# Optimization experiments

Measured on AMD Instinct MI355X. Metric: run time of the kernel, lower is better.

## Reference

```python
import jax, jax.numpy as jnp
import numpy as np

N = 100000      # total nodes (100 graphs x 1000 nodes each)
G = 100         # graphs per batch
F_IN = 12       # node_features (temporal window)
F_OUT = 32      # DCRNN hidden size (hardcoded in module)
K = 5           # diffusion (Chebyshev) steps (hardcoded)
C = 4           # num_classes
E = 16 * N      # edges: ring (N) + random (15N)


def setup_inputs() -> dict:
    key = jax.random.key(0)
    ks = jax.random.split(key, 12)
    x = jax.random.normal(ks[0], (N, F_IN), dtype=jnp.float32)
    ring = jnp.arange(N, dtype=jnp.int32)
    src = jnp.concatenate([ring, jax.random.randint(ks[1], (15 * N,), 0, N, dtype=jnp.int32)])
    dst = jnp.concatenate([(ring + 1) % N, jax.random.randint(ks[2], (15 * N,), 0, N, dtype=jnp.int32)])
    edge_index = jnp.stack([src, dst])  # [2, E]
    edge_weight = jax.random.uniform(ks[3], (E,), dtype=jnp.float32, minval=0.1, maxval=1.0)
    batch = (jnp.arange(N, dtype=jnp.int32) * G) // N  # sorted graph ids, 1000 nodes per graph
    s = 0.1
    return dict(
        x=x, edge_index=edge_index, edge_weight=edge_weight, batch=batch,
        W_z=jax.random.normal(ks[4], (2, K, F_IN + F_OUT, F_OUT), jnp.float32) * s,
        b_z=jax.random.normal(ks[5], (F_OUT,), jnp.float32) * s,
        W_r=jax.random.normal(ks[6], (2, K, F_IN + F_OUT, F_OUT), jnp.float32) * s,
        b_r=jax.random.normal(ks[7], (F_OUT,), jnp.float32) * s,
        W_h=jax.random.normal(ks[8], (2, K, F_IN + F_OUT, F_OUT), jnp.float32) * s,
        b_h=jax.random.normal(ks[9], (F_OUT,), jnp.float32) * s,
        W_lin=jax.random.normal(ks[10], (F_OUT, C), jnp.float32) * s,
        b_lin=jax.random.normal(ks[11], (C,), jnp.float32) * s,
    )


def reference(x, edge_index, edge_weight, batch, W_z, b_z, W_r, b_r, W_h, b_h, W_lin, b_lin):
    row, col = edge_index[0], edge_index[1]
    # weighted in/out degrees (to_dense_adj sums duplicate edges, same as segment_sum)
    deg_out_inv = 1.0 / jax.ops.segment_sum(edge_weight, row, num_segments=N)
    deg_in_inv = 1.0 / jax.ops.segment_sum(edge_weight, col, num_segments=N)
    norm_out = deg_out_inv[row][:, None]  # per-edge 1/deg_out(src)
    norm_in = deg_in_inv[row][:, None]    # per-edge 1/deg_in(src), as in DConv

    def prop_fwd(h):  # out[dst] += h[src]/deg_out[src]
        return jax.ops.segment_sum(norm_out * h[row], col, num_segments=N)

    def prop_rev(h):  # reverse (transposed) diffusion: out[src] += h[dst]/deg_in[src]
        return jax.ops.segment_sum(norm_in * h[col], row, num_segments=N)

    def dconv(Xc, W, b):
        # Chebyshev diffusion conv, W: [2, K, F_in+F_out, F_out]
        H = Xc @ (W[0, 0] + W[1, 0])
        T1o, T1i = prop_fwd(Xc), prop_rev(Xc)
        H = H + T1o @ W[0, 1] + T1i @ W[1, 1]
        T0o = T0i = Xc
        for k in range(2, K):
            T2o = 2.0 * prop_fwd(T1o) - T0o
            T2i = 2.0 * prop_rev(T1i) - T0i
            H = H + T2o @ W[0, k] + T2i @ W[1, k]
            T0o, T1o = T1o, T2o
            T0i, T1i = T1i, T2i
        return H + b

    # GRU gating with zero-initialized hidden state (H=None in module)
    Hst = jnp.zeros((N, F_OUT), x.dtype)
    XH = jnp.concatenate([x, Hst], axis=1)
    Z = jax.nn.sigmoid(dconv(XH, W_z, b_z))
    R = jax.nn.sigmoid(dconv(XH, W_r, b_r))
    XRH = jnp.concatenate([x, R * Hst], axis=1)
    H_tilde = jnp.tanh(dconv(XRH, W_h, b_h))
    H = Z * Hst + (1.0 - Z) * H_tilde

    h = jax.nn.relu(H) @ W_lin + b_lin            # [N, C]
    sums = jax.ops.segment_sum(h, batch, num_segments=G)
    counts = jax.ops.segment_sum(jnp.ones((N,), h.dtype), batch, num_segments=G)
    return sums / counts[:, None]                 # global_mean_pool -> [G, C]
```

## Files before the change

### kernel.cpp

```cpp
#include <hip/hip_runtime.h>
#include <math.h>

#define NN    100000
#define GG    100
#define FIN   12
#define FOUT  32
#define KD    5
#define CC    4
#define EE    1600000
#define ROWS  108
#define NBF   782
#define NBINS 1564
#define NBC   512
#define CHUNK 3125
#define TOTR  (2 * CHUNK)
#define NSEG  (NBINS * NBC)
#define SUBMAX 3072

__device__ __forceinline__ unsigned bfr(float f) {
    unsigned u = __float_as_uint(f);
    return (u + 0x7FFFu + ((u >> 16) & 1u)) >> 16;
}
__device__ __forceinline__ unsigned pack2(float a, float b) {
    return bfr(a) | (bfr(b) << 16);
}
#define BLO(u) __uint_as_float((u) << 16)
#define BHI(u) __uint_as_float((u) & 0xFFFF0000u)

__device__ __forceinline__ int chunk_of_block(int b) {
    return ((b & 7) << 6) | (b >> 3);
}


__global__ __launch_bounds__(512) void k_hist(const int* __restrict__ ei,
                                              int* __restrict__ hist_g) {
    __shared__ int hist[NBINS];
    for (int i = threadIdx.x; i < NBINS; i += 512) hist[i] = 0;
    __syncthreads();
    int chunk = chunk_of_block(blockIdx.x);
    int lo = chunk * CHUNK, hi = lo + CHUNK;
    for (int e = lo + threadIdx.x; e < hi; e += 512) {
        int s = ei[e], d = ei[EE + e];
        atomicAdd(&hist[d >> 7], 1);
        atomicAdd(&hist[NBF + (s >> 7)], 1);
    }
    __syncthreads();
    for (int i = threadIdx.x; i < NBINS; i += 512)
        hist_g[i * NBC + chunk] = hist[i];
}

__global__ __launch_bounds__(1024) void k_scan1(
        int* __restrict__ g, int* __restrict__ bsum,
        const float* __restrict__ Wz_in, const float* __restrict__ Wh_in,
        float* __restrict__ Wz, float* __restrict__ Wh,
        const float* __restrict__ b_lin, float* __restrict__ out,
        const float* __restrict__ x, uint2* __restrict__ xb) {
    __shared__ int sh[1024];
    int t = threadIdx.x;
    int i = blockIdx.x * 1024 + t;
    int v = g[i];
    sh[t] = v;
    __syncthreads();
    for (int d = 1; d < 1024; d <<= 1) {
        int x2 = sh[t];
        if (t >= d) x2 += sh[t - d];
        __syncthreads();
        sh[t] = x2;
        __syncthreads();
    }
    g[i] = sh[t] - v;
    if (t == 1023) bsum[blockIdx.x] = sh[1023];

    if (i < 2 * ROWS * FOUT) {
        int sel = i / (ROWS * FOUT);
        int rem = i - sel * ROWS * FOUT;
        int r = rem / FOUT;
        int f = rem - r * FOUT;
        int b = r / 12;
        int ii = r - b * 12;
        const float* Ws = sel ? Wh_in : Wz_in;
        float vv;
        if (b == 0)
            vv = Ws[(0 * KD + 0) * 44 * 32 + ii * 32 + f] + Ws[(1 * KD + 0) * 44 * 32 + ii * 32 + f];
        else if (b <= 4)
            vv = Ws[(0 * KD + b) * 44 * 32 + ii * 32 + f];
        else
            vv = Ws[(1 * KD + (b - 4)) * 44 * 32 + ii * 32 + f];
        (sel ? Wh : Wz)[r * FOUT + f] = vv;
    }
    int u = i - 2 * ROWS * FOUT;
    if (u >= 0 && u < GG * CC) out[u] = b_lin[u & 3];
    if (i < 3 * NN) {
        int n = i / 3, c = i - n * 3;
        float4 vf = *(const float4*)(x + (size_t)n * FIN + c * 4);
        xb[(size_t)n * 3 + c] = make_uint2(pack2(vf.x, vf.y), pack2(vf.z, vf.w));
    }
}

__global__ __launch_bounds__(1024) void k_scan3(int* __restrict__ g,
                                                const int* __restrict__ bsum,
                                                int* __restrict__ off,
                                                int* __restrict__ off_node) {
    __shared__ int sh[1024];
    int t = threadIdx.x;
    sh[t] = (t < blockIdx.x) ? bsum[t] : 0;
    __syncthreads();
    for (int d = 512; d > 0; d >>= 1) {
        if (t < d) sh[t] += sh[t + d];
        __syncthreads();
    }
    int base = sh[0];
    int i = blockIdx.x * 1024 + t;
    int v = g[i] + base;
    g[i] = v;
    if ((i & (NBC - 1)) == 0) off[i / NBC] = v;
    if (i == 0) { off[NBINS] = 2 * EE; off_node[2 * NN] = 2 * EE; }
}

__global__ __launch_bounds__(512) void k_place(const int* __restrict__ ei,
                                               const float* __restrict__ ew,
                                               const int* __restrict__ base_g,
                                               int2* __restrict__ recA) {
    __shared__ int2 ldsrec[TOTR];
    __shared__ int  lofs[NBINS];
    __shared__ int  cur[NBINS];
    __shared__ int  sbase[NBINS];
    __shared__ unsigned short binof[TOTR];
    int* psum = (int*)binof;
    int t = threadIdx.x;
    int chunk = chunk_of_block(blockIdx.x);

    for (int bin = t; bin < NBINS; bin += 512) {
        int b0 = base_g[bin * NBC + chunk];
        int b1;
        if (chunk < NBC - 1)      b1 = base_g[bin * NBC + chunk + 1];
        else if (bin < NBINS - 1) b1 = base_g[(bin + 1) * NBC];
        else                      b1 = 2 * EE;
        sbase[bin] = b0;
        lofs[bin] = b1 - b0;
        cur[bin] = 0;
    }
    __syncthreads();

    int i0 = t * 4;
    int v0 = 0, v1 = 0, v2 = 0, v3 = 0;
    if (i0 + 0 < NBINS) v0 = lofs[i0];
    if (i0 + 1 < NBINS) v1 = lofs[i0 + 1];
    if (i0 + 2 < NBINS) v2 = lofs[i0 + 2];
    if (i0 + 3 < NBINS) v3 = lofs[i0 + 3];
    int s = v0 + v1 + v2 + v3;
    psum[t] = s;
    __syncthreads();
    for (int d = 1; d < 512; d <<= 1) {
        int x = psum[t];
        if (t >= d) x += psum[t - d];
        __syncthreads();
        psum[t] = x;
        __syncthreads();
    }
    int run = psum[t] - s;
    __syncthreads();
    if (i0 + 0 < NBINS) { lofs[i0]     = run; run += v0; }
    if (i0 + 1 < NBINS) { lofs[i0 + 1] = run; run += v1; }
    if (i0 + 2 < NBINS) { lofs[i0 + 2] = run; run += v2; }
    if (i0 + 3 < NBINS) { lofs[i0 + 3] = run; run += v3; }
    __syncthreads();

    int lo = chunk * CHUNK;
    for (int e = lo + t; e < lo + CHUNK; e += 512) {
        int s2 = ei[e], d2 = ei[EE + e];
        float w = ew[e];
        int bf = d2 >> 7;
        int pf = lofs[bf] + atomicAdd(&cur[bf], 1);
        ldsrec[pf] = make_int2(s2 | ((d2 & 127) << 17), __float_as_int(w));
        binof[pf] = (unsigned short)bf;
        int br = NBF + (s2 >> 7);
        int pr = lofs[br] + atomicAdd(&cur[br], 1);
        ldsrec[pr] = make_int2(d2 | ((s2 & 127) << 17), __float_as_int(w));
        binof[pr] = (unsigned short)br;
    }
    __syncthreads();

    for (int i = t; i < TOTR; i += 512) {
        int b = binof[i];
        recA[sbase[b] + (i - lofs[b])] = ldsrec[i];
    }
}

__global__ __launch_bounds__(256) void k_subcsr(
        const int* __restrict__ off, const int2* __restrict__ recA,
        const float* __restrict__ x,
        int* __restrict__ off_node, int* __restrict__ rec2,
        float* __restrict__ dinv_in, float* __restrict__ dinv_out,
        uint2* __restrict__ gA) {
    __shared__ int2  seg[SUBMAX];
    __shared__ int   hist[128];
    __shared__ int   lofs[128];
    __shared__ int   cur[128];
    __shared__ float wsum[128];
    __shared__ float dl[128];
    int b = blockIdx.x;
    int t = threadIdx.x;
    if (t < 128) { hist[t] = 0; wsum[t] = 0.f; }
    __syncthreads();
    int e0 = off[b], e1 = off[b + 1];
    int cnt = e1 - e0;
    bool stg = (cnt <= SUBMAX);
    if (stg) {
        for (int i = t; i < cnt; i += 256) {
            int2 r = recA[e0 + i];
            seg[i] = r;
            int loc = r.x >> 17;
            atomicAdd(&hist[loc], 1);
            atomicAdd(&wsum[loc], __int_as_float(r.y));
        }
    } else {
        for (int i = t; i < cnt; i += 256) {
            int2 r = recA[e0 + i];
            int loc = r.x >> 17;
            atomicAdd(&hist[loc], 1);
            atomicAdd(&wsum[loc], __int_as_float(r.y));
        }
    }
    __syncthreads();
    if (t < 128) lofs[t] = hist[t];
    __syncthreads();
    for (int d = 1; d < 128; d <<= 1) {
        int v = 0;
        if (t < 128 && t >= d) v = lofs[t - d];
        __syncthreads();
        if (t < 128) lofs[t] += v;
        __syncthreads();
    }
    bool rev = b >= NBF;
    int base = (rev ? b - NBF : b) * 128;
    if (t < 128) {
        int ex = lofs[t] - hist[t];
        lofs[t] = ex;
        cur[t] = 0;
        int node = base + t;
        if (node < NN) {
            off_node[(rev ? NN : 0) + node] = e0 + ex;
            float inv = 1.f / wsum[t];
            dl[t] = inv;
            if (rev) dinv_out[node] = inv;
            else     dinv_in[node]  = inv;
        }
    }
    __syncthreads();
    if (stg) {
        for (int i = t; i < cnt; i += 256) {
            int rx = seg[i].x;
            int loc = rx >> 17;
            int pos = e0 + lofs[loc] + atomicAdd(&cur[loc], 1);
            rec2[pos] = rx & 0x1FFFF;
        }
    } else {
        for (int i = t; i < cnt; i += 256) {
            int rx = recA[e0 + i].x;
            int loc = rx >> 17;
            int pos = e0 + lofs[loc] + atomicAdd(&cur[loc], 1);
            rec2[pos] = rx & 0x1FFFF;
        }
    }
    if (rev) {
        __syncthreads();
        for (int i = t; i < 128 * 3; i += 256) {
            int loc = i / 3, cc = i - loc * 3;
            int node = base + loc;
            if (node < NN) {
                float4 v = *(const float4*)(x + (size_t)node * FIN + cc * 4);
                float sc = dl[loc];
                gA[(size_t)node * 3 + cc] =
                    make_uint2(pack2(v.x * sc, v.y * sc), pack2(v.z * sc, v.w * sc));
            }
        }
    }
}

#define LREC 2048
__global__ __launch_bounds__(256) void k_gather(
        const int* __restrict__ off_node, const int* __restrict__ rec2,
        const uint2* __restrict__ gIn, const uint2* __restrict__ hIn,
        const uint2* __restrict__ prevF, const uint2* __restrict__ prevR,
        const float* __restrict__ dinv_in, const float* __restrict__ dinv_out,
        uint2* __restrict__ outF, uint2* __restrict__ outR,
        uint2* __restrict__ gOut, float c) {
    __shared__ int lrec[LREC];
    int xcd = blockIdx.x & 7;
    int grp = blockIdx.x >> 3;
    bool rev = xcd >= 4;
    int dbase = rev ? NN : 0;
    int ub = (grp * 4 + (xcd & 3)) * 256;
    int lin = ub + threadIdx.x;

    int u1 = ub + 255; if (u1 > 3 * NN - 1) u1 = 3 * NN - 1;
    int node0 = ub / 3, node1 = u1 / 3;
    int w0 = off_node[dbase + node0];
    int w1 = off_node[dbase + node1 + 1];
    int wn = w1 - w0;
    bool useLds = (wn <= LREC);
    if (useLds) {
        for (int i = threadIdx.x; i < wn; i += 256) lrec[i] = rec2[w0 + i];
    }
    __syncthreads();

    if (lin < 3 * NN) {
        int node = lin / 3;
        int ch = lin - node * 3;
        int i0 = dbase + node;
        int e0 = off_node[i0], e1 = off_node[i0 + 1];
        const uint2* in = rev ? hIn : gIn;

        float ax = 0.f, ay = 0.f, az = 0.f, aw = 0.f;
        float bx = 0.f, by = 0.f, bz = 0.f, bw = 0.f;
        if (useLds) {
            int a0 = e0 - w0, a1 = e1 - w0;
            int e = a0;
            for (; e + 7 < a1; e += 8) {
                int n0 = lrec[e],     n1 = lrec[e + 1], n2 = lrec[e + 2], n3 = lrec[e + 3];
                int n4 = lrec[e + 4], n5 = lrec[e + 5], n6 = lrec[e + 6], n7 = lrec[e + 7];
                uint2 v0 = in[(size_t)n0 * 3 + ch];
                uint2 v1 = in[(size_t)n1 * 3 + ch];
                uint2 v2 = in[(size_t)n2 * 3 + ch];
                uint2 v3 = in[(size_t)n3 * 3 + ch];
                uint2 v4 = in[(size_t)n4 * 3 + ch];
                uint2 v5 = in[(size_t)n5 * 3 + ch];
                uint2 v6 = in[(size_t)n6 * 3 + ch];
                uint2 v7 = in[(size_t)n7 * 3 + ch];
                ax += BLO(v0.x); ay += BHI(v0.x); az += BLO(v0.y); aw += BHI(v0.y);
                bx += BLO(v1.x); by += BHI(v1.x); bz += BLO(v1.y); bw += BHI(v1.y);
                ax += BLO(v2.x); ay += BHI(v2.x); az += BLO(v2.y); aw += BHI(v2.y);
                bx += BLO(v3.x); by += BHI(v3.x); bz += BLO(v3.y); bw += BHI(v3.y);
                ax += BLO(v4.x); ay += BHI(v4.x); az += BLO(v4.y); aw += BHI(v4.y);
                bx += BLO(v5.x); by += BHI(v5.x); bz += BLO(v5.y); bw += BHI(v5.y);
                ax += BLO(v6.x); ay += BHI(v6.x); az += BLO(v6.y); aw += BHI(v6.y);
                bx += BLO(v7.x); by += BHI(v7.x); bz += BLO(v7.y); bw += BHI(v7.y);
            }
            for (; e < a1; ++e) {
                int n0 = lrec[e];
                uint2 v0 = in[(size_t)n0 * 3 + ch];
                ax += BLO(v0.x); ay += BHI(v0.x); az += BLO(v0.y); aw += BHI(v0.y);
            }
        } else {
            for (int e = e0; e < e1; ++e) {
                int n0 = rec2[e];
                uint2 v0 = in[(size_t)n0 * 3 + ch];
                ax += BLO(v0.x); ay += BHI(v0.x); az += BLO(v0.y); aw += BHI(v0.y);
            }
        }
        ax += bx; ay += by; az += bz; aw += bw;

        float sc = rev ? c * dinv_in[node] : c;
        ax *= sc; ay *= sc; az *= sc; aw *= sc;

        size_t o = (size_t)node * 3 + ch;
        if (prevF) {
            uint2 p = (rev ? prevR : prevF)[o];
            ax -= BLO(p.x); ay -= BHI(p.x); az -= BLO(p.y); aw -= BHI(p.y);
        }
        (rev ? outR : outF)[o] = make_uint2(pack2(ax, ay), pack2(az, aw));
        if (!rev && gOut) {
            float g = dinv_out[node];
            gOut[o] = make_uint2(pack2(g * ax, g * ay), pack2(g * az, g * aw));
        }
    }
}


#define SEGN  50
#define NSEGB 20
#define FREC  1280
__global__ __launch_bounds__(256) void k_fused(
        const float* __restrict__ x, const uint2* __restrict__ TS2,
        const int* __restrict__ off_node, const int* __restrict__ rec2,
        const uint2* __restrict__ gB, const float* __restrict__ dinv_in,
        const float* __restrict__ Wz, const float* __restrict__ Wh,
        const float* __restrict__ bz, const float* __restrict__ bh,
        const float* __restrict__ Wlin, float* __restrict__ out) {
    __shared__ float rows[64][13];
    __shared__ float red[256 * CC];
    __shared__ int   frec[FREC];
    int g = blockIdx.x / NSEGB;
    int seg = blockIdx.x - g * NSEGB;
    int base = g * 1000 + seg * SEGN;
    int tid = threadIdx.x;
    int lane = tid & 63;
    int wave = tid >> 6;
    int f0 = __builtin_amdgcn_readfirstlane(wave * 8);
    bool act = lane < SEGN;

    const uint2* T2o = TS2 + (size_t)1 * NN * 3;
    const uint2* T2i = TS2 + (size_t)5 * NN * 3;
    const uint2* T3i = TS2 + (size_t)6 * NN * 3;

    float az0[8], ah0[8];
#pragma unroll
    for (int fi = 0; fi < 8; ++fi) {
        az0[fi] = bz[f0 + fi];
        ah0[fi] = bh[f0 + fi];
    }

    for (int b = 0; b < 9; ++b) {
        __syncthreads();
        if (b == 0) {
            const float* src = x + (size_t)base * FIN;
            if (tid < 150) {
                float4 v = *(const float4*)(src + tid * 4);
                int e = tid * 4;
                int n0 = e / 12,       i0 = e - n0 * 12;       rows[n0][i0] = v.x;
                int n1 = (e + 1) / 12, i1 = (e + 1) - n1 * 12; rows[n1][i1] = v.y;
                int n2 = (e + 2) / 12, i2 = (e + 2) - n2 * 12; rows[n2][i2] = v.z;
                int n3 = (e + 3) / 12, i3 = (e + 3) - n3 * 12; rows[n3][i3] = v.w;
            }
        } else if (b == 4 || b == 8) {
            bool revd = (b == 8);
            int dbase = revd ? NN : 0;
            const uint2* gin  = revd ? T3i : gB;
            const uint2* prev = revd ? T2i : T2o;
            int w0 = off_node[dbase + base];
            int w1 = off_node[dbase + base + SEGN];
            int wn = w1 - w0;
            bool useLds = (wn <= FREC);
            if (useLds) {
                for (int i = tid; i < wn; i += 256) frec[i] = rec2[w0 + i];
            }
            __syncthreads();
            if (tid < 150) {
                int n = tid / 3, cc = tid - n * 3;
                int node = base + n;
                int e0 = off_node[dbase + node], e1 = off_node[dbase + node + 1];
                float ax = 0.f, ay = 0.f, az = 0.f, aw = 0.f;
                float bx2 = 0.f, by2 = 0.f, bz2 = 0.f, bw2 = 0.f;
                if (useLds) {
                    int a0 = e0 - w0, a1 = e1 - w0;
                    int e = a0;
                    for (; e + 7 < a1; e += 8) {
                        int n0 = frec[e],     n1 = frec[e + 1], n2 = frec[e + 2], n3 = frec[e + 3];
                        int n4 = frec[e + 4], n5 = frec[e + 5], n6 = frec[e + 6], n7 = frec[e + 7];
                        uint2 v0 = gin[(size_t)n0 * 3 + cc];
                        uint2 v1 = gin[(size_t)n1 * 3 + cc];
                        uint2 v2 = gin[(size_t)n2 * 3 + cc];
                        uint2 v3 = gin[(size_t)n3 * 3 + cc];
                        uint2 v4 = gin[(size_t)n4 * 3 + cc];
                        uint2 v5 = gin[(size_t)n5 * 3 + cc];
                        uint2 v6 = gin[(size_t)n6 * 3 + cc];
                        uint2 v7 = gin[(size_t)n7 * 3 + cc];
                        ax += BLO(v0.x); ay += BHI(v0.x); az += BLO(v0.y); aw += BHI(v0.y);
                        bx2 += BLO(v1.x); by2 += BHI(v1.x); bz2 += BLO(v1.y); bw2 += BHI(v1.y);
                        ax += BLO(v2.x); ay += BHI(v2.x); az += BLO(v2.y); aw += BHI(v2.y);
                        bx2 += BLO(v3.x); by2 += BHI(v3.x); bz2 += BLO(v3.y); bw2 += BHI(v3.y);
                        ax += BLO(v4.x); ay += BHI(v4.x); az += BLO(v4.y); aw += BHI(v4.y);
                        bx2 += BLO(v5.x); by2 += BHI(v5.x); bz2 += BLO(v5.y); bw2 += BHI(v5.y);
                        ax += BLO(v6.x); ay += BHI(v6.x); az += BLO(v6.y); aw += BHI(v6.y);
                        bx2 += BLO(v7.x); by2 += BHI(v7.x); bz2 += BLO(v7.y); bw2 += BHI(v7.y);
                    }
                    for (; e < a1; ++e) {
                        uint2 v = gin[(size_t)frec[e] * 3 + cc];
                        ax += BLO(v.x); ay += BHI(v.x); az += BLO(v.y); aw += BHI(v.y);
                    }
                } else {
                    for (int e = e0; e < e1; ++e) {
                        uint2 v = gin[(size_t)rec2[e] * 3 + cc];
                        ax += BLO(v.x); ay += BHI(v.x); az += BLO(v.y); aw += BHI(v.y);
                    }
                }
                ax += bx2; ay += by2; az += bz2; aw += bw2;
                float sc = revd ? 2.f * dinv_in[node] : 2.f;
                uint2 p = prev[(size_t)node * 3 + cc];
                rows[n][cc * 4 + 0] = ax * sc - BLO(p.x);
                rows[n][cc * 4 + 1] = ay * sc - BHI(p.x);
                rows[n][cc * 4 + 2] = az * sc - BLO(p.y);
                rows[n][cc * 4 + 3] = aw * sc - BHI(p.y);
            }
        } else {
            const uint2* Tb = TS2 + (size_t)(b - 1) * NN * 3;
            if (tid < 150) {
                int n = tid / 3, cc = tid - n * 3;
                uint2 v = Tb[(size_t)(base + n) * 3 + cc];
                rows[n][cc * 4 + 0] = BLO(v.x);
                rows[n][cc * 4 + 1] = BHI(v.x);
                rows[n][cc * 4 + 2] = BLO(v.y);
                rows[n][cc * 4 + 3] = BHI(v.y);
            }
        }
        __syncthreads();
        const float* wzr = Wz + b * 12 * FOUT + f0;
        const float* whr = Wh + b * 12 * FOUT + f0;
#pragma unroll
        for (int i = 0; i < FIN; ++i) {
            float v0 = rows[lane][i];
#pragma unroll
            for (int fi = 0; fi < 8; ++fi) {
                float wz = wzr[i * FOUT + fi];
                float wh = whr[i * FOUT + fi];
                az0[fi] = fmaf(v0, wz, az0[fi]);
                ah0[fi] = fmaf(v0, wh, ah0[fi]);
            }
        }
    }

    float o[CC] = {0.f, 0.f, 0.f, 0.f};
    if (act) {
#pragma unroll
        for (int fi = 0; fi < 8; ++fi) {
            float z = 1.f / (1.f + __expf(-az0[fi]));
            float e2 = __expf(2.f * ah0[fi]);
            float th = 1.f - 2.f / (e2 + 1.f);
            float hv = fmaxf((1.f - z) * th, 0.f);
#pragma unroll
            for (int c = 0; c < CC; ++c) o[c] = fmaf(hv, Wlin[(f0 + fi) * 4 + c], o[c]);
        }
    }

#pragma unroll
    for (int c = 0; c < CC; ++c) red[tid * CC + c] = o[c];
    __syncthreads();
    for (int st = 128; st > 0; st >>= 1) {
        if (tid < st) {
#pragma unroll
            for (int c = 0; c < CC; ++c) red[tid * CC + c] += red[(tid + st) * CC + c];
        }
        __syncthreads();
    }
    if (tid == 0) {
#pragma unroll
        for (int c = 0; c < CC; ++c) atomicAdd(out + g * CC + c, red[c] * 0.001f);
    }
}


extern "C" void kernel_launch(void* const* d_in, const int* in_sizes, int n_in,
                              void* d_out, int out_size, void* d_ws, size_t ws_size,
                              hipStream_t stream) {
    const float* x     = (const float*)d_in[0];
    const int*   ei    = (const int*)d_in[1];
    const float* ew    = (const float*)d_in[2];
    const float* W_z   = (const float*)d_in[4];
    const float* b_z   = (const float*)d_in[5];
    const float* W_h   = (const float*)d_in[8];
    const float* b_h   = (const float*)d_in[9];
    const float* W_lin = (const float*)d_in[10];
    const float* b_lin = (const float*)d_in[11];
    float* out = (float*)d_out;

    int*   rec2     = (int*)d_ws;
    unsigned* TSb   = (unsigned*)(rec2 + 2 * (size_t)EE);
    int2*  recA     = (int2*)TSb;
    int*   hist_g   = rec2;
    int*   bsumS    = rec2 + NSEG;
    unsigned* gAu   = TSb + (size_t)8 * NN * 6 + 1600000;
    unsigned* gBu   = gAu + (size_t)NN * 6;
    unsigned* xbu   = gBu + (size_t)NN * 6;
    float* dinv_in  = (float*)(xbu + (size_t)NN * 6);
    float* dinv_out = dinv_in + NN;
    float* Wz       = dinv_out + NN;
    float* Wh       = Wz + ROWS * FOUT;
    int*   off      = (int*)(Wh + ROWS * FOUT);
    int*   off_node = off + NBINS + 1;

    uint2* TS2 = (uint2*)TSb;
    uint2* T1o = TS2 + (size_t)0 * NN * 3;
    uint2* T2o = TS2 + (size_t)1 * NN * 3;
    uint2* T3o = TS2 + (size_t)2 * NN * 3;
    uint2* T1i = TS2 + (size_t)4 * NN * 3;
    uint2* T2i = TS2 + (size_t)5 * NN * 3;
    uint2* T3i = TS2 + (size_t)6 * NN * 3;
    uint2* gA = (uint2*)gAu;
    uint2* gB = (uint2*)gBu;
    uint2* xb = (uint2*)xbu;

    dim3 B(256);
    int nbG = 2344;
    int nbScan = NSEG / 1024;

    k_hist<<<NBC, 512, 0, stream>>>(ei, hist_g);
    k_scan1<<<nbScan, 1024, 0, stream>>>(hist_g, bsumS, W_z, W_h, Wz, Wh, b_lin, out, x, xb);
    k_scan3<<<nbScan, 1024, 0, stream>>>(hist_g, bsumS, off, off_node);
    k_place<<<NBC, 512, 0, stream>>>(ei, ew, hist_g, recA);
    k_subcsr<<<NBINS, B, 0, stream>>>(off, recA, x, off_node, rec2, dinv_in, dinv_out, gA);

    k_gather<<<nbG, B, 0, stream>>>(off_node, rec2, gA, xb,  nullptr, nullptr, dinv_in, dinv_out, T1o, T1i, gB, 1.f);
    k_gather<<<nbG, B, 0, stream>>>(off_node, rec2, gB, T1i, xb,      xb,      dinv_in, dinv_out, T2o, T2i, gA, 2.f);
    k_gather<<<nbG, B, 0, stream>>>(off_node, rec2, gA, T2i, T1o,     T1i,     dinv_in, dinv_out, T3o, T3i, gB, 2.f);

    k_fused<<<NSEGB * GG, B, 0, stream>>>(x, TS2, off_node, rec2, gB, dinv_in,
                                          Wz, Wh, b_z, b_h, W_lin, out);
}
```

Baseline: 299.9 us.

## Warp-specialize fused head kernel with producer/consumer double-buffered rows

The final fused kernel now uses 512-thread blocks covering 250 nodes instead of 50. Four producer waves load or gather the next basis block into one of two LDS row buffers while four consumer waves accumulate the projection for the current block, each consumer handling four nodes. This overlaps the gather latency with the FMA work, cuts the block count, and raises per-thread register use. The gather portion is spread over fewer total threads, which may limit parallelism in the memory-bound gather steps.

```diff
diff --git a/kernel.cpp b/kernel.cpp
--- a/kernel.cpp
+++ b/kernel.cpp
@@ -368,155 +368,178 @@
 }
 
 
-#define SEGN  50
-#define NSEGB 20
-#define FREC  1280
-__global__ __launch_bounds__(256) void k_fused(
+#define SEGN  250
+#define NSEGB 4
+#define FREC  5120
+__global__ __launch_bounds__(512) void k_fused(
         const float* __restrict__ x, const uint2* __restrict__ TS2,
         const int* __restrict__ off_node, const int* __restrict__ rec2,
         const uint2* __restrict__ gB, const float* __restrict__ dinv_in,
         const float* __restrict__ Wz, const float* __restrict__ Wh,
         const float* __restrict__ bz, const float* __restrict__ bh,
         const float* __restrict__ Wlin, float* __restrict__ out) {
-    __shared__ float rows[64][13];
-    __shared__ float red[256 * CC];
+    __shared__ float rows[2][256][13];
+    __shared__ float red[512 * CC];
     __shared__ int   frec[FREC];
-    int g = blockIdx.x / NSEGB;
-    int seg = blockIdx.x - g * NSEGB;
+    int g = blockIdx.x >> 2;
+    int seg = blockIdx.x & 3;
     int base = g * 1000 + seg * SEGN;
     int tid = threadIdx.x;
     int lane = tid & 63;
     int wave = tid >> 6;
-    int f0 = __builtin_amdgcn_readfirstlane(wave * 8);
-    bool act = lane < SEGN;
+    bool cons = wave < 4;
+    int pid = tid - 256;
+    int f0 = __builtin_amdgcn_readfirstlane((wave & 3) * 8);
 
     const uint2* T2o = TS2 + (size_t)1 * NN * 3;
     const uint2* T2i = TS2 + (size_t)5 * NN * 3;
     const uint2* T3i = TS2 + (size_t)6 * NN * 3;
 
-    float az0[8], ah0[8];
+    float az0[8], ah0[8], az1[8], ah1[8], az2[8], ah2[8], az3[8], ah3[8];
 #pragma unroll
     for (int fi = 0; fi < 8; ++fi) {
-        az0[fi] = bz[f0 + fi];
-        ah0[fi] = bh[f0 + fi];
-    }
+        float vz = bz[f0 + fi], vh = bh[f0 + fi];
+        az0[fi] = vz; ah0[fi] = vh; az1[fi] = vz; ah1[fi] = vh;
+        az2[fi] = vz; ah2[fi] = vh; az3[fi] = vz; ah3[fi] = vh;
+    }
+
+    if (!cons) {
+        const float* src = x + (size_t)base * FIN;
+        for (int q = pid; q < 750; q += 256) {
+            float4 v = *(const float4*)(src + q * 4);
+            int e = q * 4;
+            int n0 = e / 12,       i0 = e - n0 * 12;       rows[0][n0][i0] = v.x;
+            int n1 = (e + 1) / 12, i1 = (e + 1) - n1 * 12; rows[0][n1][i1] = v.y;
+            int n2 = (e + 2) / 12, i2 = (e + 2) - n2 * 12; rows[0][n2][i2] = v.z;
+            int n3 = (e + 3) / 12, i3 = (e + 3) - n3 * 12; rows[0][n3][i3] = v.w;
+        }
+    }
+    __syncthreads();
 
     for (int b = 0; b < 9; ++b) {
-        __syncthreads();
-        if (b == 0) {
-            const float* src = x + (size_t)base * FIN;
-            if (tid < 150) {
-                float4 v = *(const float4*)(src + tid * 4);
-                int e = tid * 4;
-                int n0 = e / 12,       i0 = e - n0 * 12;       rows[n0][i0] = v.x;
-                int n1 = (e + 1) / 12, i1 = (e + 1) - n1 * 12; rows[n1][i1] = v.y;
-                int n2 = (e + 2) / 12, i2 = (e + 2) - n2 * 12; rows[n2][i2] = v.z;
-                int n3 = (e + 3) / 12, i3 = (e + 3) - n3 * 12; rows[n3][i3] = v.w;
-            }
-        } else if (b == 4 || b == 8) {
-            bool revd = (b == 8);
+        int nb = b + 1;
+        int cur = b & 1, nxt = nb & 1;
+        if (nb == 4 || nb == 8) {
+            bool revd = (nb == 8);
             int dbase = revd ? NN : 0;
-            const uint2* gin  = revd ? T3i : gB;
-            const uint2* prev = revd ? T2i : T2o;
             int w0 = off_node[dbase + base];
             int w1 = off_node[dbase + base + SEGN];
             int wn = w1 - w0;
             bool useLds = (wn <= FREC);
             if (useLds) {
-                for (int i = tid; i < wn; i += 256) frec[i] = rec2[w0 + i];
+                for (int i = tid; i < wn; i += 512) frec[i] = rec2[w0 + i];
             }
             __syncthreads();
-            if (tid < 150) {
-                int n = tid / 3, cc = tid - n * 3;
-                int node = base + n;
-                int e0 = off_node[dbase + node], e1 = off_node[dbase + node + 1];
-                float ax = 0.f, ay = 0.f, az = 0.f, aw = 0.f;
-                float bx2 = 0.f, by2 = 0.f, bz2 = 0.f, bw2 = 0.f;
-                if (useLds) {
-                    int a0 = e0 - w0, a1 = e1 - w0;
-                    int e = a0;
-                    for (; e + 7 < a1; e += 8) {
-                        int n0 = frec[e],     n1 = frec[e + 1], n2 = frec[e + 2], n3 = frec[e + 3];
-                        int n4 = frec[e + 4], n5 = frec[e + 5], n6 = frec[e + 6], n7 = frec[e + 7];
-                        uint2 v0 = gin[(size_t)n0 * 3 + cc];
-                        uint2 v1 = gin[(size_t)n1 * 3 + cc];
-                        uint2 v2 = gin[(size_t)n2 * 3 + cc];
-                        uint2 v3 = gin[(size_t)n3 * 3 + cc];
-                        uint2 v4 = gin[(size_t)n4 * 3 + cc];
-                        uint2 v5 = gin[(size_t)n5 * 3 + cc];
-                        uint2 v6 = gin[(size_t)n6 * 3 + cc];
-                        uint2 v7 = gin[(size_t)n7 * 3 + cc];
-                        ax += BLO(v0.x); ay += BHI(v0.x); az += BLO(v0.y); aw += BHI(v0.y);
-                        bx2 += BLO(v1.x); by2 += BHI(v1.x); bz2 += BLO(v1.y); bw2 += BHI(v1.y);
-                        ax += BLO(v2.x); ay += BHI(v2.x); az += BLO(v2.y); aw += BHI(v2.y);
-                        bx2 += BLO(v3.x); by2 += BHI(v3.x); bz2 += BLO(v3.y); bw2 += BHI(v3.y);
-                        ax += BLO(v4.x); ay += BHI(v4.x); az += BLO(v4.y); aw += BHI(v4.y);
-                        bx2 += BLO(v5.x); by2 += BHI(v5.x); bz2 += BLO(v5.y); bw2 += BHI(v5.y);
-                        ax += BLO(v6.x); ay += BHI(v6.x); az += BLO(v6.y); aw += BHI(v6.y);
-                        bx2 += BLO(v7.x); by2 += BHI(v7.x); bz2 += BLO(v7.y); bw2 += BHI(v7.y);
+            if (!cons) {
+                const uint2* gin  = revd ? T3i : gB;
+                const uint2* prev = revd ? T2i : T2o;
+                for (int item = pid; item < 750; item += 256) {
+                    int n = item / 3, cc = item - n * 3;
+                    int node = base + n;
+                    int e0 = off_node[dbase + node], e1 = off_node[dbase + node + 1];
+                    float ax = 0.f, ay = 0.f, az = 0.f, aw = 0.f;
+                    float bx2 = 0.f, by2 = 0.f, bz2 = 0.f, bw2 = 0.f;
+                    if (useLds) {
+                        int a0 = e0 - w0, a1 = e1 - w0;
+                        int e = a0;
+                        for (; e + 7 < a1; e += 8) {
+                            int n0 = frec[e],     n1 = frec[e + 1], n2 = frec[e + 2], n3 = frec[e + 3];
+                            int n4 = frec[e + 4], n5 = frec[e + 5], n6 = frec[e + 6], n7 = frec[e + 7];
+                            uint2 v0 = gin[(size_t)n0 * 3 + cc];
+                            uint2 v1 = gin[(size_t)n1 * 3 + cc];
+                            uint2 v2 = gin[(size_t)n2 * 3 + cc];
+                            uint2 v3 = gin[(size_t)n3 * 3 + cc];
+                            uint2 v4 = gin[(size_t)n4 * 3 + cc];
+                            uint2 v5 = gin[(size_t)n5 * 3 + cc];
+                            uint2 v6 = gin[(size_t)n6 * 3 + cc];
+                            uint2 v7 = gin[(size_t)n7 * 3 + cc];
+                            ax += BLO(v0.x); ay += BHI(v0.x); az += BLO(v0.y); aw += BHI(v0.y);
+                            bx2 += BLO(v1.x); by2 += BHI(v1.x); bz2 += BLO(v1.y); bw2 += BHI(v1.y);
+                            ax += BLO(v2.x); ay += BHI(v2.x); az += BLO(v2.y); aw += BHI(v2.y);
+                            bx2 += BLO(v3.x); by2 += BHI(v3.x); bz2 += BLO(v3.y); bw2 += BHI(v3.y);
+                            ax += BLO(v4.x); ay += BHI(v4.x); az += BLO(v4.y); aw += BHI(v4.y);
+                            bx2 += BLO(v5.x); by2 += BHI(v5.x); bz2 += BLO(v5.y); bw2 += BHI(v5.y);
+                            ax += BLO(v6.x); ay += BHI(v6.x); az += BLO(v6.y); aw += BHI(v6.y);
+                            bx2 += BLO(v7.x); by2 += BHI(v7.x); bz2 += BLO(v7.y); bw2 += BHI(v7.y);
+                        }
+                        for (; e < a1; ++e) {
+                            uint2 v = gin[(size_t)frec[e] * 3 + cc];
+                            ax += BLO(v.x); ay += BHI(v.x); az += BLO(v.y); aw += BHI(v.y);
+                        }
+                    } else {
+                        for (int e = e0; e < e1; ++e) {
+                            uint2 v = gin[(size_t)rec2[e] * 3 + cc];
+                            ax += BLO(v.x); ay += BHI(v.x); az += BLO(v.y); aw += BHI(v.y);
+                        }
                     }
-                    for (; e < a1; ++e) {
-                        uint2 v = gin[(size_t)frec[e] * 3 + cc];
-                        ax += BLO(v.x); ay += BHI(v.x); az += BLO(v.y); aw += BHI(v.y);
-                    }
-                } else {
-                    for (int e = e0; e < e1; ++e) {
-                        uint2 v = gin[(size_t)rec2[e] * 3 + cc];
-                        ax += BLO(v.x); ay += BHI(v.x); az += BLO(v.y); aw += BHI(v.y);
-                    }
+                    ax += bx2; ay += by2; az += bz2; aw += bw2;
+                    float sc = revd ? 2.f * dinv_in[node] : 2.f;
+                    uint2 p = prev[(size_t)node * 3 + cc];
+                    rows[nxt][n][cc * 4 + 0] = ax * sc - BLO(p.x);
+                    rows[nxt][n][cc * 4 + 1] = ay * sc - BHI(p.x);
+                    rows[nxt][n][cc * 4 + 2] = az * sc - BLO(p.y);
+                    rows[nxt][n][cc * 4 + 3] = aw * sc - BHI(p.y);
                 }
-                ax += bx2; ay += by2; az += bz2; aw += bw2;
-                float sc = revd ? 2.f * dinv_in[node] : 2.f;
-                uint2 p = prev[(size_t)node * 3 + cc];
-                rows[n][cc * 4 + 0] = ax * sc - BLO(p.x);
-                rows[n][cc * 4 + 1] = ay * sc - BHI(p.x);
-                rows[n][cc * 4 + 2] = az * sc - BLO(p.y);
-                rows[n][cc * 4 + 3] = aw * sc - BHI(p.y);
-            }
-        } else {
-            const uint2* Tb = TS2 + (size_t)(b - 1) * NN * 3;
-            if (tid < 150) {
-                int n = tid / 3, cc = tid - n * 3;
-                uint2 v = Tb[(size_t)(base + n) * 3 + cc];
-                rows[n][cc * 4 + 0] = BLO(v.x);
-                rows[n][cc * 4 + 1] = BHI(v.x);
-                rows[n][cc * 4 + 2] = BLO(v.y);
-                rows[n][cc * 4 + 3] = BHI(v.y);
-            }
-        }
-        __syncthreads();
-        const float* wzr = Wz + b * 12 * FOUT + f0;
-        const float* whr = Wh + b * 12 * FOUT + f0;
-#pragma unroll
-        for (int i = 0; i < FIN; ++i) {
-            float v0 = rows[lane][i];
+            }
+        } else if (nb <= 8) {
+            if (!cons) {
+                const uint2* Tb = TS2 + (size_t)(nb - 1) * NN * 3;
+                for (int item = pid; item < 750; item += 256) {
+                    int n = item / 3, cc = item - n * 3;
+                    uint2 v = Tb[(size_t)(base + n) * 3 + cc];
+                    rows[nxt][n][cc * 4 + 0] = BLO(v.x);
+                    rows[nxt][n][cc * 4 + 1] = BHI(v.x);
+                    rows[nxt][n][cc * 4 + 2] = BLO(v.y);
+                    rows[nxt][n][cc * 4 + 3] = BHI(v.y);
+                }
+            }
+        }
+        if (cons) {
+            const float* wzr = Wz + b * 12 * FOUT + f0;
+            const float* whr = Wh + b * 12 * FOUT + f0;
+#pragma unroll
+            for (int i = 0; i < FIN; ++i) {
+                float v0 = rows[cur][lane][i];
+                float v1 = rows[cur][lane + 64][i];
+                float v2 = rows[cur][lane + 128][i];
+                float v3 = rows[cur][lane + 192][i];
+#pragma unroll
+                for (int fi = 0; fi < 8; ++fi) {
+                    float wz = wzr[i * FOUT + fi];
+                    float wh = whr[i * FOUT + fi];
+                    az0[fi] = fmaf(v0, wz, az0[fi]); ah0[fi] = fmaf(v0, wh, ah0[fi]);
+                    az1[fi] = fmaf(v1, wz, az1[fi]); ah1[fi] = fmaf(v1, wh, ah1[fi]);
+                    az2[fi] = fmaf(v2, wz, az2[fi]); ah2[fi] = fmaf(v2, wh, ah2[fi]);
+                    az3[fi] = fmaf(v3, wz, az3[fi]); ah3[fi] = fmaf(v3, wh, ah3[fi]);
+                }
+            }
+        }
+        __syncthreads();
+    }
+
+    float o[CC] = {0.f, 0.f, 0.f, 0.f};
+    if (cons) {
+        auto actacc = [&](const float* azp, const float* ahp) {
 #pragma unroll
             for (int fi = 0; fi < 8; ++fi) {
-                float wz = wzr[i * FOUT + fi];
-                float wh = whr[i * FOUT + fi];
-                az0[fi] = fmaf(v0, wz, az0[fi]);
-                ah0[fi] = fmaf(v0, wh, ah0[fi]);
-            }
-        }
-    }
-
-    float o[CC] = {0.f, 0.f, 0.f, 0.f};
-    if (act) {
-#pragma unroll
-        for (int fi = 0; fi < 8; ++fi) {
-            float z = 1.f / (1.f + __expf(-az0[fi]));
-            float e2 = __expf(2.f * ah0[fi]);
-            float th = 1.f - 2.f / (e2 + 1.f);
-            float hv = fmaxf((1.f - z) * th, 0.f);
-#pragma unroll
-            for (int c = 0; c < CC; ++c) o[c] = fmaf(hv, Wlin[(f0 + fi) * 4 + c], o[c]);
-        }
+                float z = 1.f / (1.f + __expf(-azp[fi]));
+                float e2 = __expf(2.f * ahp[fi]);
+                float th = 1.f - 2.f / (e2 + 1.f);
+                float hv = fmaxf((1.f - z) * th, 0.f);
+#pragma unroll
+                for (int c = 0; c < CC; ++c) o[c] = fmaf(hv, Wlin[(f0 + fi) * 4 + c], o[c]);
+            }
+        };
+        actacc(az0, ah0);
+        actacc(az1, ah1);
+        actacc(az2, ah2);
+        if (lane < 58) actacc(az3, ah3);
     }
 
 #pragma unroll
     for (int c = 0; c < CC; ++c) red[tid * CC + c] = o[c];
     __syncthreads();
-    for (int st = 128; st > 0; st >>= 1) {
+    for (int st = 256; st > 0; st >>= 1) {
         if (tid < st) {
 #pragma unroll
             for (int c = 0; c < CC; ++c) red[tid * CC + c] += red[(tid + st) * CC + c];
@@ -584,6 +607,6 @@
     k_gather<<<nbG, B, 0, stream>>>(off_node, rec2, gB, T1i, xb,      xb,      dinv_in, dinv_out, T2o, T2i, gA, 2.f);
     k_gather<<<nbG, B, 0, stream>>>(off_node, rec2, gA, T2i, T1o,     T1i,     dinv_in, dinv_out, T3o, T3i, gB, 2.f);
 
-    k_fused<<<NSEGB * GG, B, 0, stream>>>(x, TS2, off_node, rec2, gB, dinv_in,
-                                          Wz, Wh, b_z, b_h, W_lin, out);
-}
+    k_fused<<<NSEGB * GG, 512, 0, stream>>>(x, TS2, off_node, rec2, gB, dinv_in,
+                                            Wz, Wh, b_z, b_h, W_lin, out);
+}
```

Result: slower. 327.5 us (+9.2%).
